# Kernel tuning notes

Hardware: AMD Instinct MI355X
Metric: run time of the kernel (lower is better)

Reference implementation:

```python
import jax, jax.numpy as jnp
import numpy as np

B, IN, H, M = 16384, 512, 512, 4096


def setup_inputs() -> dict:
    key = jax.random.key(0)
    ks = jax.random.split(key, 8)
    s_in = 1.0 / np.sqrt(IN + H)
    return {
        "input_tensor": jax.random.normal(ks[0], (B, IN), jnp.float32),
        "hidden": jax.random.normal(ks[1], (B, H), jnp.float32),
        "cell": jax.random.normal(ks[2], (B, H), jnp.float32),
        # fused gate weights: columns = [input, forget, cell, output] gates
        "W_gates": jax.random.normal(ks[3], (IN + H, 4 * H), jnp.float32) * s_in,
        "b_gates": jnp.zeros((4 * H,), jnp.float32),
        "W_attn": jax.random.normal(ks[4], (H, M), jnp.float32) / np.sqrt(H),
        "b_attn": jnp.zeros((M,), jnp.float32),
        "memory_matrix": jax.random.normal(ks[5], (M, H), jnp.float32) * np.sqrt(2.0 / (M + H)),
    }


def reference(input_tensor, hidden, cell, W_gates, b_gates, W_attn, b_attn, memory_matrix):
    combined = jnp.concatenate([input_tensor, hidden], axis=1)        # (B, IN+H)
    gates = combined @ W_gates + b_gates                              # (B, 4H)
    i_g, f_g, c_g, o_g = jnp.split(gates, 4, axis=1)
    i_g = jax.nn.sigmoid(i_g)
    f_g = jax.nn.sigmoid(f_g)
    c_g = jnp.tanh(c_g)
    o_g = jax.nn.sigmoid(o_g)
    attn = jax.nn.softmax(hidden @ W_attn + b_attn, axis=1)           # (B, M)
    memory_read = attn @ memory_matrix                                # (B, H)
    new_cell = f_g * cell + i_g * c_g + 0.1 * memory_read
    new_hidden = o_g * jnp.tanh(new_cell)
    return (new_hidden, new_cell, attn)
```

## Files before the change

### kernel.cpp

```cpp
#include <hip/hip_runtime.h>
#include <hip/hip_bf16.h>
#include <math.h>

typedef __bf16 bf16_t;
typedef bf16_t bf16x8 __attribute__((ext_vector_type(8)));
typedef float  f32x4  __attribute__((ext_vector_type(4)));

static constexpr int Bn = 16384;
static constexpr int Hn = 512;

__device__ __forceinline__ float sigm(float x) { return 1.0f / (1.0f + __expf(-x)); }

typedef __attribute__((address_space(3))) void lds_void;
typedef const __attribute__((address_space(1))) void gl_void;

__device__ __forceinline__ void glds16(const void* g, void* l) {
    __builtin_amdgcn_global_load_lds((gl_void*)g, (lds_void*)l, 16, 0, 0);
}

__global__ void convert_comb(const float* __restrict__ inp, const float* __restrict__ hid,
                             bf16_t* __restrict__ comb)
{
    size_t t = (size_t)blockIdx.x * blockDim.x + threadIdx.x;
    size_t r = t >> 7;
    int c8 = (int)(t & 127);
    const float* src = (c8 < 64) ? (inp + r * 512 + c8 * 8) : (hid + r * 512 + (c8 - 64) * 8);
    float4 a = ((const float4*)src)[0];
    float4 b = ((const float4*)src)[1];
    bf16x8 o;
    o[0] = (bf16_t)a.x; o[1] = (bf16_t)a.y; o[2] = (bf16_t)a.z; o[3] = (bf16_t)a.w;
    o[4] = (bf16_t)b.x; o[5] = (bf16_t)b.y; o[6] = (bf16_t)b.z; o[7] = (bf16_t)b.w;
    *(bf16x8*)(comb + t * 8) = o;
}

__global__ void transpose_all(const float* __restrict__ Wg, bf16_t* __restrict__ WgT,
                              const float* __restrict__ Wa, bf16_t* __restrict__ WaT,
                              const float* __restrict__ Mem, bf16_t* __restrict__ MemT)
{
    __shared__ float tile[32][33];
    int b = blockIdx.x;
    const float* src; bf16_t* dst; int R, C, gx;
    if (b < 2048)      { src = Wg;  dst = WgT;  R = 1024; C = 2048; gx = 64; }
    else if (b < 4096) { b -= 2048; src = Wa;  dst = WaT;  R = 512;  C = 4096; gx = 128; }
    else               { b -= 4096; src = Mem; dst = MemT; R = 4096; C = 512;  gx = 16; }
    const int x0 = (b % gx) * 32, y0 = (b / gx) * 32;
    const int tx = threadIdx.x & 31, ty = threadIdx.x >> 5;
#pragma unroll
    for (int i = 0; i < 32; i += 8)
        tile[ty + i][tx] = src[(size_t)(y0 + ty + i) * C + x0 + tx];
    __syncthreads();
#pragma unroll
    for (int i = 0; i < 32; i += 8)
        dst[(size_t)(x0 + ty + i) * R + y0 + tx] = (bf16_t)tile[tx][ty + i];
}

template<int EPI>
__global__ __launch_bounds__(512)
void gemm_w8(const bf16_t* __restrict__ A, int lda,
             const bf16_t* __restrict__ Bt, int ldb,
             const float* __restrict__ bias, int K, int N,
             bf16_t* __restrict__ bout, int ost)
{
    __shared__ __align__(16) bf16_t sA[128 * 64];
    __shared__ __align__(16) bf16_t sB[256 * 64];

    const int tid = threadIdx.x, lane = tid & 63, wid = tid >> 6;
    const int wr = wid >> 2, wc = wid & 3;

    const int nwg = gridDim.x;
    int bid = (blockIdx.x & 7) * (nwg >> 3) + (blockIdx.x >> 3);
    const int cbn = N >> 8;
    const int row0 = (bid / cbn) * 128, col0 = (bid % cbn) * 256;

    f32x4 acc[4][4] = {};
    const int nk = K >> 6;
    const int l15 = lane & 15, kq = lane >> 4;

    for (int kt = 0; kt < nk; ++kt) {
        const int k0 = kt << 6;
        {
            const int slot = (lane & 7) ^ (lane >> 3);
#pragma unroll
            for (int t = 0; t < 2; ++t) {
                const int c8 = wid * 2 + t;
                const int r = c8 * 8 + (lane >> 3);
                glds16(A + (size_t)(row0 + r) * lda + k0 + slot * 8, sA + c8 * 512);
            }
#pragma unroll
            for (int t = 0; t < 4; ++t) {
                const int c8 = wid * 4 + t;
                const int r = c8 * 8 + (lane >> 3);
                glds16(Bt + (size_t)(col0 + r) * ldb + k0 + slot * 8, sB + c8 * 512);
            }
        }
        __syncthreads();
#pragma unroll
        for (int ks = 0; ks < 2; ++ks) {
            bf16x8 af[4], bfr[4];
            const int slot = (ks * 4 + kq) ^ (l15 & 7);
#pragma unroll
            for (int j = 0; j < 4; ++j) {
                const int rb = wc * 64 + j * 16 + l15;
                bfr[j] = *(const bf16x8*)&sB[rb * 64 + slot * 8];
                const int ra = wr * 64 + j * 16 + l15;
                af[j] = *(const bf16x8*)&sA[ra * 64 + slot * 8];
            }
#pragma unroll
            for (int i = 0; i < 4; ++i)
#pragma unroll
                for (int j = 0; j < 4; ++j)
                    acc[i][j] = __builtin_amdgcn_mfma_f32_16x16x32_bf16(af[i], bfr[j], acc[i][j], 0, 0, 0);
        }
        __syncthreads();
    }

    const int lr = (lane >> 4) * 4, lc = lane & 15;
#pragma unroll
    for (int i = 0; i < 4; ++i) {
#pragma unroll
        for (int j = 0; j < 4; ++j) {
#pragma unroll
            for (int r = 0; r < 4; ++r) {
                const int grow = row0 + wr * 64 + i * 16 + lr + r;
                const int gcol = col0 + wc * 64 + j * 16 + lc;
                float v = acc[i][j][r] + bias[gcol];
                if constexpr (EPI == 0) {
                    const float a = ((gcol >> 9) == 2) ? tanhf(v) : sigm(v);
                    bout[(size_t)grow * 2048 + gcol] = (bf16_t)a;
                } else {
                    bout[(size_t)grow * ost + gcol] = (bf16_t)v;
                }
            }
        }
    }
}

__global__ __launch_bounds__(512)
void gemm3k(const bf16_t* __restrict__ Ap, int astride,
            const bf16_t* __restrict__ MemT,
            const bf16_t* __restrict__ gates, const float* __restrict__ cell,
            float* __restrict__ fout)
{
    __shared__ __align__(16) bf16_t sA[64 * 64];
    __shared__ __align__(16) bf16_t sB[256 * 64];

    const int tid = threadIdx.x, lane = tid & 63, wid = tid >> 6;
    const int wr = wid >> 2, wc = wid & 3;

    int bid = (blockIdx.x & 7) * 64 + (blockIdx.x >> 3);
    const int row0 = (bid >> 1) * 64, col0 = (bid & 1) * 256;

    f32x4 acc[2][4] = {};
    const int l15 = lane & 15, kq = lane >> 4;

    for (int kt = 0; kt < 64; ++kt) {
        const int k0 = kt << 6;
        const int slot = (lane & 7) ^ (lane >> 3);
        {
            const int c8 = wid;
            const int r = c8 * 8 + (lane >> 3);
            glds16(Ap + (size_t)(row0 + r) * astride + k0 + slot * 8, sA + c8 * 512);
        }
#pragma unroll
        for (int t = 0; t < 4; ++t) {
            const int c8 = wid * 4 + t;
            const int r = c8 * 8 + (lane >> 3);
            glds16(MemT + (size_t)(col0 + r) * 4096 + k0 + slot * 8, sB + c8 * 512);
        }
        __syncthreads();
#pragma unroll
        for (int ks = 0; ks < 2; ++ks) {
            bf16x8 af[2], bfr[4];
            const int sl = (ks * 4 + kq) ^ (l15 & 7);
#pragma unroll
            for (int j = 0; j < 4; ++j) {
                const int rb = wc * 64 + j * 16 + l15;
                bfr[j] = *(const bf16x8*)&sB[rb * 64 + sl * 8];
            }
#pragma unroll
            for (int i = 0; i < 2; ++i) {
                const int ra = wr * 32 + i * 16 + l15;
                af[i] = *(const bf16x8*)&sA[ra * 64 + sl * 8];
            }
#pragma unroll
            for (int i = 0; i < 2; ++i)
#pragma unroll
                for (int j = 0; j < 4; ++j)
                    acc[i][j] = __builtin_amdgcn_mfma_f32_16x16x32_bf16(af[i], bfr[j], acc[i][j], 0, 0, 0);
        }
        __syncthreads();
    }

    const int lr = (lane >> 4) * 4, lc = lane & 15;
#pragma unroll
    for (int i = 0; i < 2; ++i) {
#pragma unroll
        for (int j = 0; j < 4; ++j) {
#pragma unroll
            for (int r = 0; r < 4; ++r) {
                const int grow = row0 + wr * 32 + i * 16 + lr + r;
                const int gcol = col0 + wc * 64 + j * 16 + lc;
                const float v = acc[i][j][r];
                const float ig = (float)gates[(size_t)grow * 2048 + gcol];
                const float fg = (float)gates[(size_t)grow * 2048 + 512 + gcol];
                const float cg = (float)gates[(size_t)grow * 2048 + 1024 + gcol];
                const float og = (float)gates[(size_t)grow * 2048 + 1536 + gcol];
                const float cv = cell[(size_t)grow * 512 + gcol];
                const float ncv = fg * cv + ig * cg + 0.1f * v;
                fout[(size_t)grow * 512 + gcol] = og * tanhf(ncv);
                fout[(size_t)Bn * Hn + (size_t)grow * 512 + gcol] = ncv;
            }
        }
    }
}

template<bool F32OUT>
__global__ void softmax_k(bf16_t* __restrict__ packed, int pstride, float* __restrict__ attnf32)
{
    const int row = blockIdx.x;
    bf16_t* lp = packed + (size_t)row * pstride;
    const int tid = threadIdx.x;

    float v[16];
    {
        bf16x8 h0 = ((const bf16x8*)lp)[tid];
        bf16x8 h1 = ((const bf16x8*)lp)[tid + 256];
#pragma unroll
        for (int k = 0; k < 8; ++k) { v[k] = (float)h0[k]; v[8 + k] = (float)h1[k]; }
    }
    float mx = v[0];
#pragma unroll
    for (int k = 1; k < 16; ++k) mx = fmaxf(mx, v[k]);
#pragma unroll
    for (int off = 32; off > 0; off >>= 1) mx = fmaxf(mx, __shfl_xor(mx, off));
    __shared__ float smx[4], ssm[4];
    if ((tid & 63) == 0) smx[tid >> 6] = mx;
    __syncthreads();
    mx = fmaxf(fmaxf(smx[0], smx[1]), fmaxf(smx[2], smx[3]));

    float sum = 0.0f;
#pragma unroll
    for (int k = 0; k < 16; ++k) { v[k] = __expf(v[k] - mx); sum += v[k]; }
#pragma unroll
    for (int off = 32; off > 0; off >>= 1) sum += __shfl_xor(sum, off);
    if ((tid & 63) == 0) ssm[tid >> 6] = sum;
    __syncthreads();
    sum = ssm[0] + ssm[1] + ssm[2] + ssm[3];

    const float inv = 1.0f / sum;
#pragma unroll
    for (int k = 0; k < 16; ++k) v[k] *= inv;

    bf16x8 o0, o1;
#pragma unroll
    for (int k = 0; k < 8; ++k) { o0[k] = (bf16_t)v[k]; o1[k] = (bf16_t)v[8 + k]; }
    ((bf16x8*)lp)[tid]       = o0;
    ((bf16x8*)lp)[tid + 256] = o1;

    if constexpr (F32OUT) {
        float* rp = attnf32 + (size_t)row * 4096;
        float4 a0 = { v[0], v[1], v[2], v[3] },   a1 = { v[4], v[5], v[6], v[7] };
        float4 a2 = { v[8], v[9], v[10], v[11] }, a3 = { v[12], v[13], v[14], v[15] };
        ((float4*)rp)[2 * tid]             = a0;
        ((float4*)rp)[2 * tid + 1]         = a1;
        ((float4*)rp)[2 * (tid + 256)]     = a2;
        ((float4*)rp)[2 * (tid + 256) + 1] = a3;
    }
}

__global__ void expand_attn(float* __restrict__ attn)
{
    const int row = blockIdx.x;
    float* rp = attn + (size_t)row * 4096;
    const int t = threadIdx.x;
    bf16x8 h0 = ((const bf16x8*)rp)[2 * t];
    bf16x8 h1 = ((const bf16x8*)rp)[2 * t + 1];
    __syncthreads();
    float4 o0 = { (float)h0[0], (float)h0[1], (float)h0[2], (float)h0[3] };
    float4 o1 = { (float)h0[4], (float)h0[5], (float)h0[6], (float)h0[7] };
    float4 o2 = { (float)h1[0], (float)h1[1], (float)h1[2], (float)h1[3] };
    float4 o3 = { (float)h1[4], (float)h1[5], (float)h1[6], (float)h1[7] };
    ((float4*)rp)[4 * t]     = o0;
    ((float4*)rp)[4 * t + 1] = o1;
    ((float4*)rp)[4 * t + 2] = o2;
    ((float4*)rp)[4 * t + 3] = o3;
}

extern "C" void kernel_launch(void* const* d_in, const int* in_sizes, int n_in,
                              void* d_out, int out_size, void* d_ws, size_t ws_size,
                              hipStream_t stream)
{
    const float* input  = (const float*)d_in[0];
    const float* hidden = (const float*)d_in[1];
    const float* cell   = (const float*)d_in[2];
    const float* Wg     = (const float*)d_in[3];
    const float* bg     = (const float*)d_in[4];
    const float* Wa     = (const float*)d_in[5];
    const float* ba     = (const float*)d_in[6];
    const float* Mem    = (const float*)d_in[7];

    float* out  = (float*)d_out;
    float* attn = out + 2ull * Bn * Hn;

    bf16_t* comb  = (bf16_t*)d_ws;
    bf16_t* WgT   = comb + (size_t)Bn * 1024;
    bf16_t* WaT   = WgT + (size_t)2048 * 1024;
    bf16_t* MemT  = WaT + (size_t)4096 * 512;
    bf16_t* gates = MemT + (size_t)512 * 4096;
    bf16_t* pws   = gates + (size_t)Bn * 2048;

    const size_t need_big = ((size_t)Bn * 1024 + 2048 * 1024 + 4096 * 512 + 512 * 4096
                             + (size_t)Bn * 2048 + (size_t)Bn * 4096) * sizeof(bf16_t);
    const bool big = ws_size >= need_big;
    bf16_t* packed = big ? pws : (bf16_t*)attn;
    const int pstride = big ? 4096 : 8192;

    convert_comb<<<8192, 256, 0, stream>>>(input, hidden, comb);
    transpose_all<<<6144, 256, 0, stream>>>(Wg, WgT, Wa, WaT, Mem, MemT);

    gemm_w8<0><<<1024, 512, 0, stream>>>(comb, 1024, WgT, 1024, bg, 1024, 2048, gates, 2048);
    gemm_w8<1><<<2048, 512, 0, stream>>>(comb + 512, 1024, WaT, 512, ba, 512, 4096,
                                         packed, pstride);

    if (big) softmax_k<true><<<Bn, 256, 0, stream>>>(packed, pstride, attn);
    else     softmax_k<false><<<Bn, 256, 0, stream>>>(packed, pstride, nullptr);

    gemm3k<<<512, 512, 0, stream>>>(packed, pstride, MemT, gates, cell, out);

    if (!big) expand_attn<<<Bn, 256, 0, stream>>>(attn);
}
```

Baseline: 462.0 us.

## Fold softmax into attention GEMM epilogue and memory-read GEMM via ones-MFMA row sums

The attention GEMM epilogue now writes exp(logits) directly, with no max subtraction. The memory-read GEMM computes the softmax denominators alongside the product using an extra MFMA against a ones vector, normalizes its output by them, and stores them. A light writer kernel then emits the normalized fp32 attention, replacing the separate softmax pass and expand kernel. Two full-row passes over the B×M logits go away, but exp without max subtraction can overflow for large logits. The gemm3f tiling also changes to 32 rows × full 512 columns, so the bf16 exp values are summed and rounded without normalization.

After: 529.2 us. 1.15x slower.

```diff
diff --git a/kernel.cpp b/kernel.cpp
--- a/kernel.cpp
+++ b/kernel.cpp
@@ -128,7 +128,7 @@
                     const float a = ((gcol >> 9) == 2) ? tanhf(v) : sigm(v);
                     bout[(size_t)grow * 2048 + gcol] = (bf16_t)a;
                 } else {
-                    bout[(size_t)grow * ost + gcol] = (bf16_t)v;
+                    bout[(size_t)grow * ost + gcol] = (bf16_t)__expf(v);
                 }
             }
         }
@@ -136,36 +136,38 @@
 }
 
 __global__ __launch_bounds__(512)
-void gemm3k(const bf16_t* __restrict__ Ap, int astride,
+void gemm3f(const bf16_t* __restrict__ E, int estride,
             const bf16_t* __restrict__ MemT,
             const bf16_t* __restrict__ gates, const float* __restrict__ cell,
-            float* __restrict__ fout)
-{
-    __shared__ __align__(16) bf16_t sA[64 * 64];
-    __shared__ __align__(16) bf16_t sB[256 * 64];
+            float* __restrict__ fout, float* __restrict__ denomBuf)
+{
+    __shared__ __align__(16) bf16_t sA[32 * 64];
+    __shared__ __align__(16) bf16_t sB[512 * 64];
 
     const int tid = threadIdx.x, lane = tid & 63, wid = tid >> 6;
-    const int wr = wid >> 2, wc = wid & 3;
-
     int bid = (blockIdx.x & 7) * 64 + (blockIdx.x >> 3);
-    const int row0 = (bid >> 1) * 64, col0 = (bid & 1) * 256;
+    const int row0 = bid * 32;
 
     f32x4 acc[2][4] = {};
+    f32x4 dacc[2] = {};
     const int l15 = lane & 15, kq = lane >> 4;
+    const int slot = (lane & 7) ^ (lane >> 3);
+
+    bf16x8 ones;
+#pragma unroll
+    for (int e = 0; e < 8; ++e) ones[e] = (bf16_t)1.0f;
 
     for (int kt = 0; kt < 64; ++kt) {
         const int k0 = kt << 6;
-        const int slot = (lane & 7) ^ (lane >> 3);
-        {
-            const int c8 = wid;
+        if (wid < 4) {
+            const int r = wid * 8 + (lane >> 3);
+            glds16(E + (size_t)(row0 + r) * estride + k0 + slot * 8, sA + wid * 512);
+        }
+#pragma unroll
+        for (int t = 0; t < 8; ++t) {
+            const int c8 = wid * 8 + t;
             const int r = c8 * 8 + (lane >> 3);
-            glds16(Ap + (size_t)(row0 + r) * astride + k0 + slot * 8, sA + c8 * 512);
-        }
-#pragma unroll
-        for (int t = 0; t < 4; ++t) {
-            const int c8 = wid * 4 + t;
-            const int r = c8 * 8 + (lane >> 3);
-            glds16(MemT + (size_t)(col0 + r) * 4096 + k0 + slot * 8, sB + c8 * 512);
+            glds16(MemT + (size_t)r * 4096 + k0 + slot * 8, sB + c8 * 512);
         }
         __syncthreads();
 #pragma unroll
@@ -174,33 +176,48 @@
             const int sl = (ks * 4 + kq) ^ (l15 & 7);
 #pragma unroll
             for (int j = 0; j < 4; ++j) {
-                const int rb = wc * 64 + j * 16 + l15;
+                const int rb = wid * 64 + j * 16 + l15;
                 bfr[j] = *(const bf16x8*)&sB[rb * 64 + sl * 8];
             }
 #pragma unroll
+            for (int i = 0; i < 2; ++i)
+                af[i] = *(const bf16x8*)&sA[(i * 16 + l15) * 64 + sl * 8];
+#pragma unroll
             for (int i = 0; i < 2; ++i) {
-                const int ra = wr * 32 + i * 16 + l15;
-                af[i] = *(const bf16x8*)&sA[ra * 64 + sl * 8];
-            }
-#pragma unroll
-            for (int i = 0; i < 2; ++i)
 #pragma unroll
                 for (int j = 0; j < 4; ++j)
                     acc[i][j] = __builtin_amdgcn_mfma_f32_16x16x32_bf16(af[i], bfr[j], acc[i][j], 0, 0, 0);
+                dacc[i] = __builtin_amdgcn_mfma_f32_16x16x32_bf16(af[i], ones, dacc[i], 0, 0, 0);
+            }
         }
         __syncthreads();
     }
 
     const int lr = (lane >> 4) * 4, lc = lane & 15;
+
+    if (wid == 0 && l15 == 0) {
+#pragma unroll
+        for (int i = 0; i < 2; ++i)
+#pragma unroll
+            for (int r = 0; r < 4; ++r)
+                denomBuf[row0 + i * 16 + lr + r] = dacc[i][r];
+    }
+
+    float invd[2][4];
+#pragma unroll
+    for (int i = 0; i < 2; ++i)
+#pragma unroll
+        for (int r = 0; r < 4; ++r) invd[i][r] = 1.0f / dacc[i][r];
+
 #pragma unroll
     for (int i = 0; i < 2; ++i) {
 #pragma unroll
         for (int j = 0; j < 4; ++j) {
 #pragma unroll
             for (int r = 0; r < 4; ++r) {
-                const int grow = row0 + wr * 32 + i * 16 + lr + r;
-                const int gcol = col0 + wc * 64 + j * 16 + lc;
-                const float v = acc[i][j][r];
+                const int grow = row0 + i * 16 + lr + r;
+                const int gcol = wid * 64 + j * 16 + lc;
+                const float v = acc[i][j][r] * invd[i][r];
                 const float ig = (float)gates[(size_t)grow * 2048 + gcol];
                 const float fg = (float)gates[(size_t)grow * 2048 + 512 + gcol];
                 const float cg = (float)gates[(size_t)grow * 2048 + 1024 + gcol];
@@ -214,72 +231,21 @@
     }
 }
 
-template<bool F32OUT>
-__global__ void softmax_k(bf16_t* __restrict__ packed, int pstride, float* __restrict__ attnf32)
+__global__ void attn_writer(const bf16_t* __restrict__ E, int estride,
+                            const float* __restrict__ denom, float* __restrict__ attn)
 {
     const int row = blockIdx.x;
-    bf16_t* lp = packed + (size_t)row * pstride;
-    const int tid = threadIdx.x;
-
-    float v[16];
-    {
-        bf16x8 h0 = ((const bf16x8*)lp)[tid];
-        bf16x8 h1 = ((const bf16x8*)lp)[tid + 256];
-#pragma unroll
-        for (int k = 0; k < 8; ++k) { v[k] = (float)h0[k]; v[8 + k] = (float)h1[k]; }
-    }
-    float mx = v[0];
-#pragma unroll
-    for (int k = 1; k < 16; ++k) mx = fmaxf(mx, v[k]);
-#pragma unroll
-    for (int off = 32; off > 0; off >>= 1) mx = fmaxf(mx, __shfl_xor(mx, off));
-    __shared__ float smx[4], ssm[4];
-    if ((tid & 63) == 0) smx[tid >> 6] = mx;
+    const bf16_t* lp = E + (size_t)row * estride;
+    const float inv = 1.0f / denom[row];
+    const int t = threadIdx.x;
+    bf16x8 a = ((const bf16x8*)lp)[2 * t];
+    bf16x8 b = ((const bf16x8*)lp)[2 * t + 1];
     __syncthreads();
-    mx = fmaxf(fmaxf(smx[0], smx[1]), fmaxf(smx[2], smx[3]));
-
-    float sum = 0.0f;
-#pragma unroll
-    for (int k = 0; k < 16; ++k) { v[k] = __expf(v[k] - mx); sum += v[k]; }
-#pragma unroll
-    for (int off = 32; off > 0; off >>= 1) sum += __shfl_xor(sum, off);
-    if ((tid & 63) == 0) ssm[tid >> 6] = sum;
-    __syncthreads();
-    sum = ssm[0] + ssm[1] + ssm[2] + ssm[3];
-
-    const float inv = 1.0f / sum;
-#pragma unroll
-    for (int k = 0; k < 16; ++k) v[k] *= inv;
-
-    bf16x8 o0, o1;
-#pragma unroll
-    for (int k = 0; k < 8; ++k) { o0[k] = (bf16_t)v[k]; o1[k] = (bf16_t)v[8 + k]; }
-    ((bf16x8*)lp)[tid]       = o0;
-    ((bf16x8*)lp)[tid + 256] = o1;
-
-    if constexpr (F32OUT) {
-        float* rp = attnf32 + (size_t)row * 4096;
-        float4 a0 = { v[0], v[1], v[2], v[3] },   a1 = { v[4], v[5], v[6], v[7] };
-        float4 a2 = { v[8], v[9], v[10], v[11] }, a3 = { v[12], v[13], v[14], v[15] };
-        ((float4*)rp)[2 * tid]             = a0;
-        ((float4*)rp)[2 * tid + 1]         = a1;
-        ((float4*)rp)[2 * (tid + 256)]     = a2;
-        ((float4*)rp)[2 * (tid + 256) + 1] = a3;
-    }
-}
-
-__global__ void expand_attn(float* __restrict__ attn)
-{
-    const int row = blockIdx.x;
     float* rp = attn + (size_t)row * 4096;
-    const int t = threadIdx.x;
-    bf16x8 h0 = ((const bf16x8*)rp)[2 * t];
-    bf16x8 h1 = ((const bf16x8*)rp)[2 * t + 1];
-    __syncthreads();
-    float4 o0 = { (float)h0[0], (float)h0[1], (float)h0[2], (float)h0[3] };
-    float4 o1 = { (float)h0[4], (float)h0[5], (float)h0[6], (float)h0[7] };
-    float4 o2 = { (float)h1[0], (float)h1[1], (float)h1[2], (float)h1[3] };
-    float4 o3 = { (float)h1[4], (float)h1[5], (float)h1[6], (float)h1[7] };
+    float4 o0 = { (float)a[0] * inv, (float)a[1] * inv, (float)a[2] * inv, (float)a[3] * inv };
+    float4 o1 = { (float)a[4] * inv, (float)a[5] * inv, (float)a[6] * inv, (float)a[7] * inv };
+    float4 o2 = { (float)b[0] * inv, (float)b[1] * inv, (float)b[2] * inv, (float)b[3] * inv };
+    float4 o3 = { (float)b[4] * inv, (float)b[5] * inv, (float)b[6] * inv, (float)b[7] * inv };
     ((float4*)rp)[4 * t]     = o0;
     ((float4*)rp)[4 * t + 1] = o1;
     ((float4*)rp)[4 * t + 2] = o2;
@@ -307,25 +273,22 @@
     bf16_t* WaT   = WgT + (size_t)2048 * 1024;
     bf16_t* MemT  = WaT + (size_t)4096 * 512;
     bf16_t* gates = MemT + (size_t)512 * 4096;
-    bf16_t* pws   = gates + (size_t)Bn * 2048;
-
-    const size_t need_big = ((size_t)Bn * 1024 + 2048 * 1024 + 4096 * 512 + 512 * 4096
-                             + (size_t)Bn * 2048 + (size_t)Bn * 4096) * sizeof(bf16_t);
+    float*  denom = (float*)(gates + (size_t)Bn * 2048);
+    bf16_t* pws   = (bf16_t*)(denom + Bn);
+
+    const size_t need_big = (size_t)((char*)(pws + (size_t)Bn * 4096) - (char*)d_ws);
     const bool big = ws_size >= need_big;
-    bf16_t* packed = big ? pws : (bf16_t*)attn;
-    const int pstride = big ? 4096 : 8192;
+    bf16_t* Ebuf = big ? pws : (bf16_t*)attn;
+    const int estride = big ? 4096 : 8192;
 
     convert_comb<<<8192, 256, 0, stream>>>(input, hidden, comb);
     transpose_all<<<6144, 256, 0, stream>>>(Wg, WgT, Wa, WaT, Mem, MemT);
 
     gemm_w8<0><<<1024, 512, 0, stream>>>(comb, 1024, WgT, 1024, bg, 1024, 2048, gates, 2048);
     gemm_w8<1><<<2048, 512, 0, stream>>>(comb + 512, 1024, WaT, 512, ba, 512, 4096,
-                                         packed, pstride);
-
-    if (big) softmax_k<true><<<Bn, 256, 0, stream>>>(packed, pstride, attn);
-    else     softmax_k<false><<<Bn, 256, 0, stream>>>(packed, pstride, nullptr);
-
-    gemm3k<<<512, 512, 0, stream>>>(packed, pstride, MemT, gates, cell, out);
-
-    if (!big) expand_attn<<<Bn, 256, 0, stream>>>(attn);
-}
+                                         Ebuf, estride);
+
+    gemm3f<<<512, 512, 0, stream>>>(Ebuf, estride, MemT, gates, cell, out, denom);
+
+    attn_writer<<<Bn, 256, 0, stream>>>(Ebuf, estride, denom, attn);
+}
```
